# Performance work log

Hardware: AMD Instinct MI355X
Metric: run time of the kernel (lower is better)

Reference implementation:

```python
import jax, jax.numpy as jnp
import numpy as np
from jax import lax

STRIDE = (1, 1)
PADDING = ((1, 1), (1, 1))
DILATION = (1, 1)
GROUPS = 1


def setup_inputs() -> dict:
    key = jax.random.key(0)
    k1, k2, k3, k4, k5 = jax.random.split(key, 5)
    # quantized int8-ish activations/weights stored as float (as in the torch module)
    x = jax.random.randint(k1, (32, 128, 56, 56), -128, 128).astype(jnp.float32)
    weight_int = jax.random.randint(k2, (256, 128, 3, 3), -128, 128).astype(jnp.float32)
    bias_int = jax.random.randint(k3, (256,), -1024, 1024).astype(jnp.float32)
    A = jax.random.randint(k4, (256,), 1, 32768)  # per-channel requant multiplier
    N = jax.random.randint(k5, (256,), 16, 25)    # per-channel shift
    return {
        "x": x,
        "weight_int": weight_int,
        "bias_int": bias_int,
        "A": A,
        "N": N,
        "out_min": 0,
        "out_max": 255,
    }


def reference(x, weight_int, bias_int, A, N, out_min, out_max):
    # emulate torch's x.int().float() truncation casts
    xq = jnp.trunc(x)
    wq = jnp.trunc(weight_int)
    bq = jnp.trunc(bias_int)
    out = lax.conv_general_dilated(
        xq, wq,
        window_strides=STRIDE,
        padding=PADDING,
        rhs_dilation=DILATION,
        feature_group_count=GROUPS,
        dimension_numbers=("NCHW", "OIHW", "NCHW"),
    )
    out = jnp.round(out + bq[None, :, None, None])
    # out *= A ; out >>= N  (torch float rshift == divide by 2**N)
    Af = A.astype(jnp.float32)[None, :, None, None]
    Nf = N.astype(jnp.float32)[None, :, None, None]
    out = out * Af / jnp.exp2(Nf)
    if out_min >= 0:
        out = jnp.clip(jnp.round(out), float(out_min), float(out_max))
    return out
```

## Files before the change

kernel.cpp:

```cpp
#include <hip/hip_runtime.h>
#include <stdint.h>

typedef int   v4i __attribute__((ext_vector_type(4)));
typedef float v4f __attribute__((ext_vector_type(4)));

#define XT_H_STRIDE (66*128)
#define XT_N_STRIDE (58*66*128)
#define XT_BYTES    (32*58*66*128)
#define WQ_BYTES    (256*1152)

__device__ __forceinline__ void gload16(const void* g, void* l) {
  __builtin_amdgcn_global_load_lds(
      (const __attribute__((address_space(1))) void*)g,
      (__attribute__((address_space(3))) void*)l, 16, 0, 0);
}

__global__ __launch_bounds__(256) void xform_x(const float* __restrict__ x,
                                               char* __restrict__ xt) {
  __shared__ int LB[56 * 33];
  int bid = blockIdx.x;
  int n  = bid / 58;
  int hp = bid - n * 58;
  int t  = threadIdx.x;
  int srch = hp - 1;
  bool rowok = (srch >= 0) && (srch < 56);
  char* dstrow = xt + (size_t)n * XT_N_STRIDE + (size_t)hp * XT_H_STRIDE;

  if (rowok) {
    const float* rb = x + ((size_t)(n * 128) * 56 + srch) * 56;
#pragma unroll
    for (int u0 = 0; u0 < 2; ++u0) {
      int u  = t + u0 * 256;
      int wb = u & 15;
      int cb = u >> 4;
      int w0 = wb * 4, ci0 = cb * 4;
      if (w0 < 56) {
        int dw[4] = {0, 0, 0, 0};
#pragma unroll
        for (int i = 0; i < 4; ++i) {
          v4f f = *(const v4f*)(rb + (size_t)(ci0 + i) * 3136 + w0);
#pragma unroll
          for (int j = 0; j < 4; ++j)
            dw[j] |= (((int)f[j]) & 255) << (8 * i);
        }
#pragma unroll
        for (int j = 0; j < 4; ++j)
          LB[(w0 + j) * 33 + cb] = dw[j];
      }
    }
    __syncthreads();
    for (int c = t; c < 528; c += 256) {
      int wp  = c >> 3;
      int cio = c & 7;
      int srw = wp - 1;
      v4i v = {0, 0, 0, 0};
      if (srw >= 0 && srw < 56) {
#pragma unroll
        for (int k = 0; k < 4; ++k) v[k] = LB[srw * 33 + cio * 4 + k];
      }
      *(v4i*)(dstrow + c * 16) = v;
    }
  } else {
    v4i z = {0, 0, 0, 0};
    for (int c = t; c < 528; c += 256) *(v4i*)(dstrow + c * 16) = z;
  }
}

__global__ __launch_bounds__(256) void xform_w(const float* __restrict__ wsrc,
                                               const int* __restrict__ Aq,
                                               const int* __restrict__ Nq,
                                               char* __restrict__ wq3,
                                               float* __restrict__ scale) {
  int idx = blockIdx.x * 256 + threadIdx.x;
  int co = idx / 1152;
  int k  = idx - co * 1152;
  int g  = k >> 7;
  int ci = k & 127;
  int kh = g / 3;
  int kw = g - 3 * kh;
  float f = wsrc[(size_t)(co * 128 + ci) * 9 + kh * 3 + kw];
  int kt    = k >> 6;
  int mhalf = co >> 7;
  int chunk = (k >> 4) & 3;
  int row   = co & 127;
  int col   = k & 15;
  wq3[(((kt * 2 + mhalf) * 4 + chunk) * 128 + row) * 16 + col] = (signed char)(int)f;
  if (idx < 256) {
    scale[idx] = (float)Aq[idx] * exp2f(-(float)Nq[idx]);
  }
}

__global__ __launch_bounds__(256, 4) void qconv_gemm(
    const char* __restrict__ xt, const char* __restrict__ wq3,
    const float* __restrict__ bias, const float* __restrict__ scale,
    const int* __restrict__ pmin, const int* __restrict__ pmax,
    float* __restrict__ out) {
  __shared__ __align__(16) char As[2][8192];
  __shared__ __align__(16) char Bs[2][8192];

  int bid = blockIdx.x;
  int xcd = bid & 7;
  int q   = bid >> 3;
  int mt  = q & 1;
  int nt  = xcd * 112 + (q >> 1);
  int n   = nt / 28;
  int ht  = nt - n * 28;
  int h0  = ht * 2;
  int m0  = mt * 128;

  int t  = threadIdx.x;
  int wv = t >> 6;
  int ln = t & 63;
  int quad = ln >> 4;
  int l16  = ln & 15;
  int wm = wv & 1, wn = wv >> 1;

  const char* xb = xt + (size_t)n * XT_N_STRIDE + (size_t)h0 * XT_H_STRIDE;

  int boffv[2];
#pragma unroll
  for (int u = 0; u < 2; ++u) {
    int s  = wv * 64 + u * 256 + ln;
    int sp = s >> 2;
    int ck = s & 3;
    boffv[u] = (sp >> 6) * XT_H_STRIDE + (sp & 63) * 128 + ((ck ^ (sp & 3)) << 4);
  }
  const int aoff = quad * 2048 + (wm * 64 + l16) * 16;
  const int boff = (wn * 64 + l16) * 64 + ((quad ^ (l16 & 3)) << 4);

  {
    const char* a0 = wq3 + (size_t)mt * 8192;
    gload16(a0 + t * 16,        As[0] + wv * 1024);
    gload16(a0 + 4096 + t * 16, As[0] + 4096 + wv * 1024);
    gload16(xb + boffv[0],      Bs[0] + wv * 1024);
    gload16(xb + boffv[1],      Bs[0] + 4096 + wv * 1024);
  }
  asm volatile("s_waitcnt vmcnt(0)" ::: "memory");
  asm volatile("s_barrier" ::: "memory");

  v4i acc[4][4];
#pragma unroll
  for (int i = 0; i < 4; ++i)
#pragma unroll
    for (int j = 0; j < 4; ++j) {
      v4i z = {0, 0, 0, 0};
      acc[i][j] = z;
    }

#pragma unroll
  for (int kt = 0; kt < 18; ++kt) {
    const int buf = kt & 1;

    asm volatile("s_barrier" ::: "memory");
    if (kt < 17) {
      const int kn  = kt + 1;
      const int gn  = kn >> 1;
      const int pn  = kn & 1;
      const int khn = gn / 3;
      const int kwn = gn - 3 * khn;
      const int koff = khn * XT_H_STRIDE + kwn * 128 + pn * 64;
      const char* an = wq3 + (size_t)(kn * 2 + mt) * 8192;
      const char* bn = xb + koff;
      gload16(an + t * 16,        As[buf ^ 1] + wv * 1024);
      gload16(an + 4096 + t * 16, As[buf ^ 1] + 4096 + wv * 1024);
      gload16(bn + boffv[0],      Bs[buf ^ 1] + wv * 1024);
      gload16(bn + boffv[1],      Bs[buf ^ 1] + 4096 + wv * 1024);
      asm volatile("s_waitcnt vmcnt(4)" ::: "memory");
    } else {
      asm volatile("s_waitcnt vmcnt(0)" ::: "memory");
    }
    asm volatile("s_barrier" ::: "memory");

    v4i a[4], b[4];
#pragma unroll
    for (int i = 0; i < 4; ++i)
      a[i] = *(const v4i*)(As[buf] + aoff + i * 256);
#pragma unroll
    for (int j = 0; j < 4; ++j)
      b[j] = *(const v4i*)(Bs[buf] + boff + j * 1024);
#pragma unroll
    for (int i = 0; i < 4; ++i)
#pragma unroll
      for (int j = 0; j < 4; ++j)
        acc[i][j] = __builtin_amdgcn_mfma_i32_16x16x64_i8(a[i], b[j], acc[i][j], 0, 0, 0);
  }

  float mn = (float)pmin[0];
  float mx = (float)pmax[0];
#pragma unroll
  for (int i = 0; i < 4; ++i) {
    int co_b = m0 + wm * 64 + i * 16 + quad * 4;
#pragma unroll
    for (int r = 0; r < 4; ++r) {
      int co = co_b + r;
      float bs = bias[co];
      float sc = scale[co];
#pragma unroll
      for (int j = 0; j < 4; ++j) {
        int sl = wn * 64 + j * 16 + l16;
        int w  = sl & 63;
        int dh = sl >> 6;
        if (w < 56) {
          float f = (float)acc[i][j][r] + bs;
          f = rintf(f * sc);
          f = fminf(fmaxf(f, mn), mx);
          out[(((size_t)n * 256 + co) * 56 + (h0 + dh)) * 56 + w] = f;
        }
      }
    }
  }
}

extern "C" void kernel_launch(void* const* d_in, const int* in_sizes, int n_in,
                              void* d_out, int out_size, void* d_ws, size_t ws_size,
                              hipStream_t stream) {
  const float* x  = (const float*)d_in[0];
  const float* w  = (const float*)d_in[1];
  const float* b  = (const float*)d_in[2];
  const int*   Aq = (const int*)d_in[3];
  const int*   Nq = (const int*)d_in[4];
  const int*   mn = (const int*)d_in[5];
  const int*   mx = (const int*)d_in[6];
  float* out = (float*)d_out;

  char*  xt    = (char*)d_ws;
  char*  wq3   = xt + XT_BYTES;
  float* scale = (float*)(wq3 + WQ_BYTES);

  hipLaunchKernelGGL(xform_x, dim3(32 * 58), dim3(256), 0, stream, x, xt);
  hipLaunchKernelGGL(xform_w, dim3(1152), dim3(256), 0, stream, w, Aq, Nq, wq3, scale);
  hipLaunchKernelGGL(qconv_gemm, dim3(1792), dim3(256), 0, stream,
                     xt, wq3, b, scale, mn, mx, out);
}
```

Before: 189.4 us.

## Widen GEMM block to all 256 output channels with 512 threads

The conv GEMM block now covers all 256 output channels with 8 wavefronts (4 along M, 2 along N) instead of two blocks of 128 channels each. The weight layout is reorganised so a K-slice of all channels is contiguous, and the grid is halved. This removes the duplicate loading of each activation tile by two blocks, at the cost of more LDS per block and fewer blocks to spread across CUs. Bias and scale are now fetched as 4-wide vectors in the epilogue.

Result: slower. 370.0 us (+95.4%).

```diff
diff --git a/kernel.cpp b/kernel.cpp
--- a/kernel.cpp
+++ b/kernel.cpp
@@ -69,7 +69,7 @@
 __global__ __launch_bounds__(256) void xform_w(const float* __restrict__ wsrc,
                                                const int* __restrict__ Aq,
                                                const int* __restrict__ Nq,
-                                               char* __restrict__ wq3,
+                                               char* __restrict__ wq4,
                                                float* __restrict__ scale) {
   int idx = blockIdx.x * 256 + threadIdx.x;
   int co = idx / 1152;
@@ -80,60 +80,53 @@
   int kw = g - 3 * kh;
   float f = wsrc[(size_t)(co * 128 + ci) * 9 + kh * 3 + kw];
   int kt    = k >> 6;
-  int mhalf = co >> 7;
   int chunk = (k >> 4) & 3;
-  int row   = co & 127;
   int col   = k & 15;
-  wq3[(((kt * 2 + mhalf) * 4 + chunk) * 128 + row) * 16 + col] = (signed char)(int)f;
+  wq4[((kt * 4 + chunk) * 256 + co) * 16 + col] = (signed char)(int)f;
   if (idx < 256) {
     scale[idx] = (float)Aq[idx] * exp2f(-(float)Nq[idx]);
   }
 }
 
-__global__ __launch_bounds__(256, 4) void qconv_gemm(
-    const char* __restrict__ xt, const char* __restrict__ wq3,
+__global__ __launch_bounds__(512, 6) void qconv_gemm(
+    const char* __restrict__ xt, const char* __restrict__ wq4,
     const float* __restrict__ bias, const float* __restrict__ scale,
     const int* __restrict__ pmin, const int* __restrict__ pmax,
     float* __restrict__ out) {
-  __shared__ __align__(16) char As[2][8192];
+  __shared__ __align__(16) char As[2][16384];
   __shared__ __align__(16) char Bs[2][8192];
 
   int bid = blockIdx.x;
   int xcd = bid & 7;
-  int q   = bid >> 3;
-  int mt  = q & 1;
-  int nt  = xcd * 112 + (q >> 1);
+  int nt  = xcd * 112 + (bid >> 3);
   int n   = nt / 28;
   int ht  = nt - n * 28;
   int h0  = ht * 2;
-  int m0  = mt * 128;
 
   int t  = threadIdx.x;
   int wv = t >> 6;
   int ln = t & 63;
   int quad = ln >> 4;
   int l16  = ln & 15;
-  int wm = wv & 1, wn = wv >> 1;
+  int wm = wv & 3, wn = wv >> 2;
 
   const char* xb = xt + (size_t)n * XT_N_STRIDE + (size_t)h0 * XT_H_STRIDE;
 
-  int boffv[2];
-#pragma unroll
-  for (int u = 0; u < 2; ++u) {
-    int s  = wv * 64 + u * 256 + ln;
+  int boffv;
+  {
+    int s  = t;
     int sp = s >> 2;
     int ck = s & 3;
-    boffv[u] = (sp >> 6) * XT_H_STRIDE + (sp & 63) * 128 + ((ck ^ (sp & 3)) << 4);
-  }
-  const int aoff = quad * 2048 + (wm * 64 + l16) * 16;
+    boffv = (sp >> 6) * XT_H_STRIDE + (sp & 63) * 128 + ((ck ^ (sp & 3)) << 4);
+  }
+  const int aoff = quad * 4096 + (wm * 64 + l16) * 16;
   const int boff = (wn * 64 + l16) * 64 + ((quad ^ (l16 & 3)) << 4);
 
   {
-    const char* a0 = wq3 + (size_t)mt * 8192;
+    const char* a0 = wq4;
     gload16(a0 + t * 16,        As[0] + wv * 1024);
-    gload16(a0 + 4096 + t * 16, As[0] + 4096 + wv * 1024);
-    gload16(xb + boffv[0],      Bs[0] + wv * 1024);
-    gload16(xb + boffv[1],      Bs[0] + 4096 + wv * 1024);
+    gload16(a0 + 8192 + t * 16, As[0] + 8192 + wv * 1024);
+    gload16(xb + boffv,         Bs[0] + wv * 1024);
   }
   asm volatile("s_waitcnt vmcnt(0)" ::: "memory");
   asm volatile("s_barrier" ::: "memory");
@@ -159,13 +152,11 @@
       const int khn = gn / 3;
       const int kwn = gn - 3 * khn;
       const int koff = khn * XT_H_STRIDE + kwn * 128 + pn * 64;
-      const char* an = wq3 + (size_t)(kn * 2 + mt) * 8192;
-      const char* bn = xb + koff;
+      const char* an = wq4 + (size_t)kn * 16384;
       gload16(an + t * 16,        As[buf ^ 1] + wv * 1024);
-      gload16(an + 4096 + t * 16, As[buf ^ 1] + 4096 + wv * 1024);
-      gload16(bn + boffv[0],      Bs[buf ^ 1] + wv * 1024);
-      gload16(bn + boffv[1],      Bs[buf ^ 1] + 4096 + wv * 1024);
-      asm volatile("s_waitcnt vmcnt(4)" ::: "memory");
+      gload16(an + 8192 + t * 16, As[buf ^ 1] + 8192 + wv * 1024);
+      gload16(xb + koff + boffv,  Bs[buf ^ 1] + wv * 1024);
+      asm volatile("s_waitcnt vmcnt(3)" ::: "memory");
     } else {
       asm volatile("s_waitcnt vmcnt(0)" ::: "memory");
     }
@@ -189,12 +180,14 @@
   float mx = (float)pmax[0];
 #pragma unroll
   for (int i = 0; i < 4; ++i) {
-    int co_b = m0 + wm * 64 + i * 16 + quad * 4;
+    int co_b = wm * 64 + i * 16 + quad * 4;
+    v4f bs4 = *(const v4f*)(bias + co_b);
+    v4f sc4 = *(const v4f*)(scale + co_b);
 #pragma unroll
     for (int r = 0; r < 4; ++r) {
       int co = co_b + r;
-      float bs = bias[co];
-      float sc = scale[co];
+      float bs = bs4[r];
+      float sc = sc4[r];
 #pragma unroll
       for (int j = 0; j < 4; ++j) {
         int sl = wn * 64 + j * 16 + l16;
@@ -224,11 +217,11 @@
   float* out = (float*)d_out;
 
   char*  xt    = (char*)d_ws;
-  char*  wq3   = xt + XT_BYTES;
-  float* scale = (float*)(wq3 + WQ_BYTES);
+  char*  wq4   = xt + XT_BYTES;
+  float* scale = (float*)(wq4 + WQ_BYTES);
 
   hipLaunchKernelGGL(xform_x, dim3(32 * 58), dim3(256), 0, stream, x, xt);
-  hipLaunchKernelGGL(xform_w, dim3(1152), dim3(256), 0, stream, w, Aq, Nq, wq3, scale);
-  hipLaunchKernelGGL(qconv_gemm, dim3(1792), dim3(256), 0, stream,
-                     xt, wq3, b, scale, mn, mx, out);
-}
+  hipLaunchKernelGGL(xform_w, dim3(1152), dim3(256), 0, stream, w, Aq, Nq, wq4, scale);
+  hipLaunchKernelGGL(qconv_gemm, dim3(896), dim3(512), 0, stream,
+                     xt, wq4, b, scale, mn, mx, out);
+}
```
